# Optimization experiments

Measured on AMD Instinct MI355X. Metric: run time of the kernel, lower is better.

## Reference

```python
import jax, jax.numpy as jnp
import numpy as np

B, N = 1, 4096
DIM, DEPTH, HEADS, DH = 768, 6, 12, 64
INNER = HEADS * DH
FF = 4 * DIM
M = 256            # FAVOR+ random features
NC = 100           # num_classes
VOCAB_OUT = NC + 2
N_POS = 50000


def setup_inputs() -> dict:
    key = jax.random.key(0)
    ks = jax.random.split(key, 16)
    s = 0.02
    d = {}
    d["methy"]  = jax.random.uniform(ks[0], (B, N), jnp.float32)
    d["chromo"] = jax.random.randint(ks[1], (B, N), 0, 30)
    d["pos"]    = jnp.sort(jax.random.randint(ks[2], (B, N), 0, N_POS), axis=-1)
    d["methy_table"]  = s * jax.random.normal(ks[3], (NC + 3, DIM), jnp.float32)
    d["chromo_table"] = s * jax.random.normal(ks[4], (30, DIM), jnp.float32)
    d["pos_table"]    = s * jax.random.normal(ks[5], (N_POS, DIM), jnp.float32)
    d["ln1_g"] = jnp.ones((DEPTH, DIM)); d["ln1_b"] = jnp.zeros((DEPTH, DIM))
    d["ln2_g"] = jnp.ones((DEPTH, DIM)); d["ln2_b"] = jnp.zeros((DEPTH, DIM))
    d["Wq"] = s * jax.random.normal(ks[6], (DEPTH, DIM, INNER), jnp.float32)
    d["Wk"] = s * jax.random.normal(ks[7], (DEPTH, DIM, INNER), jnp.float32)
    d["Wv"] = s * jax.random.normal(ks[8], (DEPTH, DIM, INNER), jnp.float32)
    d["Wo"] = s * jax.random.normal(ks[9], (DEPTH, INNER, DIM), jnp.float32)
    d["bo"] = jnp.zeros((DEPTH, DIM))
    d["W1"] = s * jax.random.normal(ks[10], (DEPTH, DIM, FF), jnp.float32)
    d["b1"] = jnp.zeros((DEPTH, FF))
    d["W2"] = s * jax.random.normal(ks[11], (DEPTH, FF, DIM), jnp.float32)
    d["b2"] = jnp.zeros((DEPTH, DIM))
    d["proj"] = jax.random.normal(ks[12], (DEPTH, M, DH), jnp.float32)  # fixed FAVOR+ projections
    d["normf_g"] = jnp.ones((DIM,)); d["normf_b"] = jnp.zeros((DIM,))
    d["Wout"] = s * jax.random.normal(ks[13], (DIM, VOCAB_OUT), jnp.float32)
    d["bout"] = jnp.zeros((VOCAB_OUT,))
    return d


def layernorm(x, g, b, eps=1e-5):
    mu = jnp.mean(x, -1, keepdims=True)
    var = jnp.var(x, -1, keepdims=True)
    return (x - mu) * jax.lax.rsqrt(var + eps) * g + b


def softmax_kernel(x, proj, is_query, eps=1e-4):
    # FAVOR+ positive random features approximating the softmax kernel.
    dnorm = x.shape[-1] ** -0.25
    ratio = proj.shape[0] ** -0.5
    xn = x * dnorm
    xd = jnp.einsum('bhnd,md->bhnm', xn, proj)            # [b,h,n,m]
    diag = 0.5 * jnp.sum(xn * xn, -1, keepdims=True)
    if is_query:
        mx = jnp.max(xd, axis=-1, keepdims=True)
    else:
        mx = jnp.max(xd, axis=(-2, -1), keepdims=True)
    return ratio * (jnp.exp(xd - diag - mx) + eps)


def favor_attention(x, mask, Wq, Wk, Wv, Wo, bo, proj):
    b, n, _ = x.shape
    def split(h):  # [b,n,inner] -> [b,h,n,d]
        return h.reshape(b, n, HEADS, DH).transpose(0, 2, 1, 3)
    q, k, v = split(x @ Wq), split(x @ Wk), split(x @ Wv)
    qf = softmax_kernel(q, proj, True)
    kf = softmax_kernel(k, proj, False)
    kf = kf * mask[:, None, :, None]                      # zero padded keys
    k_sum = kf.sum(axis=-2)                               # [b,h,m]
    d_inv = 1.0 / jnp.einsum('bhnm,bhm->bhn', qf, k_sum)
    ctx = jnp.einsum('bhnm,bhnd->bhmd', kf, v)            # [b,h,m,d]
    o = jnp.einsum('bhnm,bhmd,bhn->bhnd', qf, ctx, d_inv)
    o = o.transpose(0, 2, 1, 3).reshape(b, n, INNER)
    return o @ Wo + bo


def reference(methy, chromo, pos, methy_table, chromo_table, pos_table,
              ln1_g, ln1_b, ln2_g, ln2_b, Wq, Wk, Wv, Wo, bo,
              W1, b1, W2, b2, proj, normf_g, normf_b, Wout, bout):
    # ContinuousEmbedding (discretized): torch.bucketize(x, boundaries[:-1]) == searchsorted left
    boundaries = jnp.concatenate([jnp.array([-2.0, -1.0], jnp.float32),
                                  jnp.linspace(0.0, 1.0, NC + 1)])
    idx = jnp.searchsorted(boundaries[:-1], methy, side='left')
    mask = methy != 0
    x = methy_table[idx] + pos_table[pos] + chromo_table[chromo]
    for l in range(DEPTH):  # pre-norm Performer blocks
        h = layernorm(x, ln1_g[l], ln1_b[l])
        x = x + favor_attention(h, mask, Wq[l], Wk[l], Wv[l], Wo[l], bo[l], proj[l])
        h = layernorm(x, ln2_g[l], ln2_b[l])
        x = x + jax.nn.gelu(h @ W1[l] + b1[l]) @ W2[l] + b2[l]
    x = layernorm(x, normf_g, normf_b)
    return x @ Wout + bout
```

## Files before the change

kernel.cpp:

```cpp
#include <hip/hip_runtime.h>
#include <cstdint>

typedef __bf16 bf16_t;
typedef __bf16 bf16x8 __attribute__((ext_vector_type(8)));
typedef __bf16 bf16x4 __attribute__((ext_vector_type(4)));
typedef float f32x4 __attribute__((ext_vector_type(4)));

#define NTOK 4096
#define DIM 768
#define DEPTH 6
#define HEADS 12
#define FFD 3072
#define VOUT 102

__device__ __forceinline__ void gl_lds16(const void* g, void* l) {
    __builtin_amdgcn_global_load_lds(
        (__attribute__((address_space(1))) void*)(g),
        (__attribute__((address_space(3))) void*)(l), 16, 0, 0);
}

__device__ __forceinline__ unsigned enc_f32(float f) {
    unsigned u = __float_as_uint(f);
    return (u & 0x80000000u) ? ~u : (u | 0x80000000u);
}
__device__ __forceinline__ float dec_f32(unsigned e) {
    unsigned u = (e & 0x80000000u) ? (e & 0x7FFFFFFFu) : ~e;
    return __uint_as_float(u);
}

template<int MODE>
__global__ __launch_bounds__(256, 2) void gemm128(
    const bf16_t* __restrict__ A, int lda, long sA,
    const bf16_t* __restrict__ B, int ldb, long sB,
    void* __restrict__ Cout, int ldc, long sC,
    int K, int nsplit,
    const float* __restrict__ bias,
    const float* __restrict__ rowscale,
    int Mvalid, int Nvalid, void* __restrict__ aux)
{
    __shared__ __align__(16) bf16_t smem[16896];
    bf16_t* As = smem;
    bf16_t* Bs = smem + 8192;
    const int bz = blockIdx.z;
    const int batch = bz / nsplit, chunk = bz % nsplit;
    A += (long)batch * sA;
    B += (long)batch * sB;
    const int t = threadIdx.x;
    const int wave = t >> 6, lane = t & 63;
    const int wm = wave >> 1, wn = wave & 1;
    const int q = lane >> 4, r = lane & 15;
    const int tileM = blockIdx.x * 128, tileN = blockIdx.y * 128;
    const int Kc = K / nsplit;
    const int k0 = chunk * Kc;

    f32x4 acc[4][4] = {};

    for (int kt = 0; kt < Kc; kt += 64) {
        const int kb = k0 + kt;
#pragma unroll
        for (int i = 0; i < 4; i++) {
            const int c = i * 256 + t;
            const int row = c >> 3, kk = (c & 7) * 8;
            gl_lds16(A + (long)(tileM + row) * lda + kb + kk, (char*)As + (i * 256 + wave * 64) * 16);
            gl_lds16(B + (long)(tileN + row) * ldb + kb + kk, (char*)Bs + (i * 256 + wave * 64) * 16);
        }
        __syncthreads();
#pragma unroll
        for (int kk = 0; kk < 64; kk += 32) {
            bf16x8 af[4], bfr[4];
#pragma unroll
            for (int i = 0; i < 4; i++)
                af[i] = *(const bf16x8*)(As + (wm * 64 + i * 16 + r) * 64 + kk + q * 8);
#pragma unroll
            for (int j = 0; j < 4; j++)
                bfr[j] = *(const bf16x8*)(Bs + (wn * 64 + j * 16 + r) * 64 + kk + q * 8);
#pragma unroll
            for (int i = 0; i < 4; i++)
#pragma unroll
                for (int j = 0; j < 4; j++)
                    acc[i][j] = __builtin_amdgcn_mfma_f32_16x16x32_bf16(af[i], bfr[j], acc[i][j], 0, 0, 0);
        }
        __syncthreads();
    }

    if (MODE == 8) {
        const float dn = 0.3535533905932738f;
        if (tileN < 1536) {
            bf16_t* QK = (bf16_t*)Cout;
            const int hcol = (tileN >> 6) + wn;
            float* dptr = (hcol < 12) ? ((float*)bias + (long)hcol * 4096)
                                      : ((float*)rowscale + (long)(hcol - 12) * 4096);
#pragma unroll
            for (int i = 0; i < 4; i++) {
#pragma unroll
                for (int e = 0; e < 4; e++) {
                    const int R = tileM + wm * 64 + i * 16 + q * 4 + e;
                    float ss = 0.0f;
#pragma unroll
                    for (int j = 0; j < 4; j++) {
                        const int Cc = tileN + wn * 64 + j * 16 + r;
                        const float v = acc[i][j][e] * dn;
                        QK[(long)R * 1536 + Cc] = (bf16_t)v;
                        ss += v * v;
                    }
                    for (int o = 8; o; o >>= 1) ss += __shfl_xor(ss, o);
                    if (r == 0) dptr[R] = 0.5f * ss;
                }
            }
        } else {
            bf16_t* VTp = (bf16_t*)aux;
            bf16_t* tile = smem;
#pragma unroll
            for (int i = 0; i < 4; i++)
#pragma unroll
                for (int j = 0; j < 4; j++)
#pragma unroll
                    for (int e = 0; e < 4; e++) {
                        const int row = wm * 64 + i * 16 + q * 4 + e;
                        const int col = wn * 64 + j * 16 + r;
                        tile[col * 130 + row] = (bf16_t)acc[i][j][e];
                    }
            __syncthreads();
            const int col = t >> 1, half = (t & 1) * 64;
            const int cg = tileN - 1536 + col;
            const int h = cg >> 6, d = cg & 63;
            bf16_t* dst = VTp + ((long)h * 128 + d) * 4096 + tileM + half;
            const bf16_t* src = tile + col * 130 + half;
#pragma unroll
            for (int u2 = 0; u2 < 64; u2 += 8)
                *(bf16x8*)(dst + u2) = *(const bf16x8*)(src + u2);
        }
        return;
    }

#pragma unroll
    for (int i = 0; i < 4; i++) {
#pragma unroll
        for (int j = 0; j < 4; j++) {
#pragma unroll
            for (int e = 0; e < 4; e++) {
                const int R = tileM + wm * 64 + i * 16 + q * 4 + e;
                const int Cc = tileN + wn * 64 + j * 16 + r;
                const float v = acc[i][j][e];
                if (MODE == 2) {
                    const float x = v + bias[Cc];
                    const float z = 0.7978845608028654f * (x + 0.044715f * x * x * x);
                    const float th = 1.0f - 2.0f / (__expf(2.0f * z) + 1.0f);
                    bf16_t* Gp = (bf16_t*)Cout;
                    Gp[(long)R * ldc + Cc] = (bf16_t)(0.5f * x * (1.0f + th));
                } else if (MODE == 4) {
                    if (R < Mvalid) {
                        float* C = (float*)Cout + (long)batch * sC;
                        atomicAdd(&C[(long)R * ldc + Cc], v);
                    }
                } else if (MODE == 5) {
                    if (Cc < Nvalid) {
                        float* C = (float*)Cout;
                        C[(long)R * ldc + Cc] = v + bias[Cc];
                    }
                } else if (MODE == 9) {
                    float* C = (float*)Cout + (long)chunk * sC;
                    C[(long)R * ldc + Cc] = v;
                }
            }
        }
    }
}

__global__ __launch_bounds__(256, 2) void qk_feat(
    const bf16_t* __restrict__ QKbf,
    const bf16_t* __restrict__ projbf,
    const float* __restrict__ diagQ,
    bf16_t* __restrict__ QF,
    unsigned* __restrict__ kmx)
{
    __shared__ __align__(16) bf16_t As[128 * 64];
    __shared__ __align__(16) bf16_t Bs[256 * 64];
    __shared__ float rmax[2][128];
    const int z = blockIdx.y;
    const bool isq = z < 12;
    const int h = isq ? z : z - 12;
    const int tileM = blockIdx.x * 128;
    const int t = threadIdx.x, wave = t >> 6, lane = t & 63;
    const int wm = wave >> 1, wn = wave & 1;
    const int q = lane >> 4, r = lane & 15;
    const bf16_t* A = QKbf + (isq ? 0 : 768) + h * 64;

#pragma unroll
    for (int i = 0; i < 4; i++) {
        const int c = i * 256 + t;
        gl_lds16(A + (long)(tileM + (c >> 3)) * 1536 + (c & 7) * 8, (char*)As + (i * 256 + wave * 64) * 16);
    }
#pragma unroll
    for (int i = 0; i < 8; i++) {
        const int c = i * 256 + t;
        gl_lds16(projbf + c * 8, (char*)Bs + (i * 256 + wave * 64) * 16);
    }
    __syncthreads();

    f32x4 acc[4][8] = {};
#pragma unroll
    for (int kk = 0; kk < 64; kk += 32) {
        bf16x8 af[4], bfr[8];
#pragma unroll
        for (int i = 0; i < 4; i++)
            af[i] = *(const bf16x8*)(As + (wm * 64 + i * 16 + r) * 64 + kk + q * 8);
#pragma unroll
        for (int j = 0; j < 8; j++)
            bfr[j] = *(const bf16x8*)(Bs + (wn * 128 + j * 16 + r) * 64 + kk + q * 8);
#pragma unroll
        for (int i = 0; i < 4; i++)
#pragma unroll
            for (int j = 0; j < 8; j++)
                acc[i][j] = __builtin_amdgcn_mfma_f32_16x16x32_bf16(af[i], bfr[j], acc[i][j], 0, 0, 0);
    }

    if (!isq) {
        float m = -3.0e38f;
#pragma unroll
        for (int i = 0; i < 4; i++)
#pragma unroll
            for (int j = 0; j < 8; j++)
#pragma unroll
                for (int e = 0; e < 4; e++) m = fmaxf(m, acc[i][j][e]);
        for (int o = 32; o; o >>= 1) m = fmaxf(m, __shfl_xor(m, o));
        if (lane == 0) rmax[0][wave] = m;
        __syncthreads();
        if (t == 0) {
            m = fmaxf(fmaxf(rmax[0][0], rmax[0][1]), fmaxf(rmax[0][2], rmax[0][3]));
            atomicMax(kmx + h, enc_f32(m));
        }
        return;
    }

#pragma unroll
    for (int i = 0; i < 4; i++) {
#pragma unroll
        for (int e = 0; e < 4; e++) {
            float m = acc[i][0][e];
#pragma unroll
            for (int j = 1; j < 8; j++) m = fmaxf(m, acc[i][j][e]);
            for (int o = 8; o; o >>= 1) m = fmaxf(m, __shfl_xor(m, o));
            if (r == 0) rmax[wn][wm * 64 + i * 16 + q * 4 + e] = m;
        }
    }
    __syncthreads();
    const float ratio = 0.0625f;
#pragma unroll
    for (int i = 0; i < 4; i++) {
#pragma unroll
        for (int e = 0; e < 4; e++) {
            const int rl = wm * 64 + i * 16 + q * 4 + e;
            const int R = tileM + rl;
            const float dg = diagQ[h * 4096 + R] + fmaxf(rmax[0][rl], rmax[1][rl]);
            bf16_t* op = QF + ((long)h * 4096 + R) * 256 + wn * 128 + r;
#pragma unroll
            for (int j = 0; j < 8; j++)
                op[j * 16] = (bf16_t)(ratio * (__expf(acc[i][j][e] - dg) + 1e-4f));
        }
    }
}

__global__ __launch_bounds__(256, 2) void kfeat_fused(
    const bf16_t* __restrict__ QKbf,
    const bf16_t* __restrict__ projbf,
    const float* __restrict__ diagK,
    const unsigned* __restrict__ kmxe,
    const float* __restrict__ maskf,
    bf16_t* __restrict__ KFT)
{
    __shared__ __align__(16) bf16_t smem[24576];
    bf16_t* As = smem;
    bf16_t* Bs = smem + 8192;
    const int h = blockIdx.y;
    const int tileM = blockIdx.x * 128;
    const int t = threadIdx.x, wave = t >> 6, lane = t & 63;
    const int wm = wave >> 1, wn = wave & 1;
    const int q = lane >> 4, r = lane & 15;
    const bf16_t* A = QKbf + 768 + h * 64;

#pragma unroll
    for (int i = 0; i < 4; i++) {
        const int c = i * 256 + t;
        gl_lds16(A + (long)(tileM + (c >> 3)) * 1536 + (c & 7) * 8, (char*)As + (i * 256 + wave * 64) * 16);
    }
#pragma unroll
    for (int i = 0; i < 8; i++) {
        const int c = i * 256 + t;
        gl_lds16(projbf + c * 8, (char*)Bs + (i * 256 + wave * 64) * 16);
    }
    __syncthreads();

    f32x4 acc[4][8] = {};
#pragma unroll
    for (int kk = 0; kk < 64; kk += 32) {
        bf16x8 af[4], bfr[8];
#pragma unroll
        for (int i = 0; i < 4; i++)
            af[i] = *(const bf16x8*)(As + (wm * 64 + i * 16 + r) * 64 + kk + q * 8);
#pragma unroll
        for (int j = 0; j < 8; j++)
            bfr[j] = *(const bf16x8*)(Bs + (wn * 128 + j * 16 + r) * 64 + kk + q * 8);
#pragma unroll
        for (int i = 0; i < 4; i++)
#pragma unroll
            for (int j = 0; j < 8; j++)
                acc[i][j] = __builtin_amdgcn_mfma_f32_16x16x32_bf16(af[i], bfr[j], acc[i][j], 0, 0, 0);
    }

    const float km = dec_f32(kmxe[h]);
    const float ratio = 0.0625f;
    float dg[4][4], mk[4][4];
#pragma unroll
    for (int i = 0; i < 4; i++)
#pragma unroll
        for (int e = 0; e < 4; e++) {
            const int R = tileM + wm * 64 + i * 16 + q * 4 + e;
            dg[i][e] = diagK[h * 4096 + R] + km;
            mk[i][e] = maskf[R];
        }

    bf16_t* tile = smem;
#pragma unroll
    for (int mhalf = 0; mhalf < 2; mhalf++) {
        __syncthreads();
        if (wn == mhalf) {
#pragma unroll
            for (int i = 0; i < 4; i++)
#pragma unroll
                for (int j = 0; j < 8; j++)
#pragma unroll
                    for (int e = 0; e < 4; e++) {
                        const int rl = wm * 64 + i * 16 + q * 4 + e;
                        const int lc = j * 16 + r;
                        tile[lc * 136 + rl] =
                            (bf16_t)(ratio * (__expf(acc[i][j][e] - dg[i][e]) + 1e-4f) * mk[i][e]);
                    }
        }
        __syncthreads();
        const int m = t >> 1, nb = (t & 1) * 64;
        bf16_t* dst = KFT + ((long)h * 256 + mhalf * 128 + m) * 4096 + tileM + nb;
        const bf16_t* src = tile + m * 136 + nb;
#pragma unroll
        for (int c = 0; c < 64; c += 8)
            *(bf16x8*)(dst + c) = *(const bf16x8*)(src + c);
    }
}

__global__ __launch_bounds__(256, 2) void pv_fused(
    const bf16_t* __restrict__ QF,
    const float* __restrict__ CTXf,
    bf16_t* __restrict__ O)
{
    __shared__ __align__(16) bf16_t As[128 * 64];
    __shared__ __align__(16) bf16_t Bs[80 * 64];
    const int h = blockIdx.y;
    const int tileM = blockIdx.x * 128;
    const int t = threadIdx.x, wave = t >> 6, lane = t & 63;
    const int wm = wave >> 1, wn = wave & 1;
    const int q = lane >> 4, r = lane & 15;

    f32x4 acc[4][5] = {};
    for (int kt = 0; kt < 256; kt += 64) {
#pragma unroll
        for (int i = 0; i < 4; i++) {
            const int c = i * 256 + t;
            gl_lds16(QF + ((long)h * 4096 + tileM + (c >> 3)) * 256 + kt + (c & 7) * 8,
                     (char*)As + (i * 256 + wave * 64) * 16);
        }
#pragma unroll
        for (int u = 0; u < 5; u++) {
            const int idx = u * 256 + t;
            const int row = idx >> 4, c4 = (idx & 15) * 4;
            const float4 v = *(const float4*)(CTXf + ((long)h * 80 + row) * 256 + kt + c4);
            bf16x4 o4; o4[0] = (bf16_t)v.x; o4[1] = (bf16_t)v.y; o4[2] = (bf16_t)v.z; o4[3] = (bf16_t)v.w;
            *(bf16x4*)(Bs + row * 64 + c4) = o4;
        }
        __syncthreads();
#pragma unroll
        for (int kk = 0; kk < 64; kk += 32) {
            bf16x8 af[4], bfr[5];
#pragma unroll
            for (int i = 0; i < 4; i++)
                af[i] = *(const bf16x8*)(As + (wm * 64 + i * 16 + r) * 64 + kk + q * 8);
#pragma unroll
            for (int j = 0; j < 5; j++)
                bfr[j] = *(const bf16x8*)(Bs + ((wn * 0 + j * 16 + r)) * 64 + kk + q * 8);
#pragma unroll
            for (int i = 0; i < 4; i++)
#pragma unroll
                for (int j = 0; j < 5; j++)
                    acc[i][j] = __builtin_amdgcn_mfma_f32_16x16x32_bf16(af[i], bfr[j], acc[i][j], 0, 0, 0);
        }
        __syncthreads();
    }
    if (wn == 1) return;
#pragma unroll
    for (int i = 0; i < 4; i++) {
#pragma unroll
        for (int e = 0; e < 4; e++) {
            const int R = tileM + wm * 64 + i * 16 + q * 4 + e;
            float den = __shfl(acc[i][4][e], lane & 0x30);
            const float dinv = 1.0f / den;
            bf16_t* op = O + (long)R * 768 + h * 64;
#pragma unroll
            for (int j = 0; j < 4; j++)
                op[j * 16 + r] = (bf16_t)(acc[i][j][e] * dinv);
        }
    }
}

__global__ void bucket_kernel(const float* __restrict__ methy, int* __restrict__ idx, float* __restrict__ maskf) {
    const int n = blockIdx.x * 256 + threadIdx.x;
    if (n >= NTOK) return;
    const float u = methy[n];
    int cnt = (int)(u > -2.0f) + (int)(u > -1.0f);
    for (int k = 0; k < 100; k++) cnt += (int)(((float)k * 0.01f) < u);
    idx[n] = cnt;
    maskf[n] = (u != 0.0f) ? 1.0f : 0.0f;
}

__global__ void embed_kernel(const int* __restrict__ idx, const int* __restrict__ pos, const int* __restrict__ chromo,
                             const float* __restrict__ mt, const float* __restrict__ pt, const float* __restrict__ ct,
                             float* __restrict__ X) {
    const int n = blockIdx.x, t = threadIdx.x;
    const float4* a = (const float4*)(mt + (long)idx[n] * DIM);
    const float4* b = (const float4*)(pt + (long)pos[n] * DIM);
    const float4* c = (const float4*)(ct + (long)chromo[n] * DIM);
    float4 rr = a[t];
    const float4 u = b[t], w = c[t];
    rr.x += u.x + w.x; rr.y += u.y + w.y; rr.z += u.z + w.z; rr.w += u.w + w.w;
    ((float4*)(X + (long)n * DIM))[t] = rr;
}

__global__ __launch_bounds__(256) void ln_fused(float* __restrict__ X,
        const float* __restrict__ D0, const float* __restrict__ D1, const float* __restrict__ rb,
        const float* __restrict__ g, const float* __restrict__ b, bf16_t* __restrict__ out) {
    const int n = blockIdx.x, t = threadIdx.x;
    float* x = X + (long)n * DIM;
    float v[3];
#pragma unroll
    for (int j = 0; j < 3; j++) {
        const int c = t + j * 256;
        float xv = x[c];
        if (D0) {
            xv += D0[(long)n * DIM + c] + D1[(long)n * DIM + c] + rb[c];
            x[c] = xv;
        }
        v[j] = xv;
    }
    float s = v[0] + v[1] + v[2];
    float s2 = v[0] * v[0] + v[1] * v[1] + v[2] * v[2];
    __shared__ float smA[4], smB[4];
    for (int o = 32; o; o >>= 1) { s += __shfl_down(s, o); s2 += __shfl_down(s2, o); }
    if ((t & 63) == 0) { smA[t >> 6] = s; smB[t >> 6] = s2; }
    __syncthreads();
    s = smA[0] + smA[1] + smA[2] + smA[3];
    s2 = smB[0] + smB[1] + smB[2] + smB[3];
    const float mu = s * (1.0f / DIM);
    const float var = s2 * (1.0f / DIM) - mu * mu;
    const float rs = rsqrtf(var + 1e-5f);
    bf16_t* op = out + (long)n * DIM;
#pragma unroll
    for (int j = 0; j < 3; j++) {
        const int c = t + j * 256;
        op[c] = (bf16_t)((v[j] - mu) * rs * g[c] + b[c]);
    }
}

__global__ __launch_bounds__(256) void transpose4(const float* __restrict__ Wq, const float* __restrict__ Wk,
        const float* __restrict__ Wv, const float* __restrict__ Wo,
        bf16_t* __restrict__ WqkvT, bf16_t* __restrict__ WoT) {
    __shared__ float tile[32][33];
    const int z = blockIdx.z, l = z >> 2, j = z & 3;
    const float* in = (j == 0 ? Wq : j == 1 ? Wk : j == 2 ? Wv : Wo) + (long)l * 768 * 768;
    bf16_t* out = (j < 3) ? WqkvT + (long)l * 2304 * 768 + (long)j * 768 * 768
                          : WoT + (long)l * 768 * 768;
    const int c0 = blockIdx.x * 32, r0 = blockIdx.y * 32;
    const int t = threadIdx.x, tx = t & 31, ty = t >> 5;
    for (int i = 0; i < 32; i += 8)
        tile[ty + i][tx] = in[(long)(r0 + ty + i) * 768 + c0 + tx];
    __syncthreads();
    for (int i = 0; i < 32; i += 8)
        out[(long)(c0 + ty + i) * 768 + r0 + tx] = (bf16_t)tile[tx][ty + i];
}

__global__ __launch_bounds__(256) void transpose_b(const float* __restrict__ in, long sIn, int R, int C,
                                                   bf16_t* __restrict__ out, long sOut, int ldo) {
    __shared__ float tile[32][33];
    in += (long)blockIdx.z * sIn;
    out += (long)blockIdx.z * sOut;
    const int c0 = blockIdx.x * 32, r0 = blockIdx.y * 32;
    const int t = threadIdx.x, tx = t & 31, ty = t >> 5;
    for (int i = 0; i < 32; i += 8) {
        const int rr = r0 + ty + i, cc = c0 + tx;
        tile[ty + i][tx] = (rr < R && cc < C) ? in[(long)rr * C + cc] : 0.0f;
    }
    __syncthreads();
    for (int i = 0; i < 32; i += 8) {
        const int cc = c0 + ty + i, rr = r0 + tx;
        if (cc < C && rr < R) out[(long)cc * ldo + rr] = (bf16_t)tile[tx][ty + i];
    }
}

__global__ void conv_kernel(const float* __restrict__ in, bf16_t* __restrict__ out, long n) {
    const long i = ((long)blockIdx.x * 256 + threadIdx.x) * 4;
    if (i >= n) return;
    const float4 v = *(const float4*)(in + i);
    bf16x4 o; o[0] = (bf16_t)v.x; o[1] = (bf16_t)v.y; o[2] = (bf16_t)v.z; o[3] = (bf16_t)v.w;
    *(bf16x4*)(out + i) = o;
}

__global__ void vtones_kernel(bf16_t* __restrict__ VT) {
    const int i = blockIdx.x * 256 + threadIdx.x;
    const int h = i >> 12, n = i & 4095;
    VT[((long)h * 128 + 64) * 4096 + n] = (bf16_t)1.0f;
}

extern "C" void kernel_launch(void* const* d_in, const int* in_sizes, int n_in,
                              void* d_out, int out_size, void* d_ws, size_t ws_size,
                              hipStream_t stream) {
    const float* methy        = (const float*)d_in[0];
    const int*   chromo       = (const int*)d_in[1];
    const int*   pos          = (const int*)d_in[2];
    const float* methy_table  = (const float*)d_in[3];
    const float* chromo_table = (const float*)d_in[4];
    const float* pos_table    = (const float*)d_in[5];
    const float* ln1_g = (const float*)d_in[6];
    const float* ln1_b = (const float*)d_in[7];
    const float* ln2_g = (const float*)d_in[8];
    const float* ln2_b = (const float*)d_in[9];
    const float* Wq = (const float*)d_in[10];
    const float* Wk = (const float*)d_in[11];
    const float* Wv = (const float*)d_in[12];
    const float* Wo = (const float*)d_in[13];
    const float* bo = (const float*)d_in[14];
    const float* W1 = (const float*)d_in[15];
    const float* b1 = (const float*)d_in[16];
    const float* W2 = (const float*)d_in[17];
    const float* b2 = (const float*)d_in[18];
    const float* proj = (const float*)d_in[19];
    const float* normf_g = (const float*)d_in[20];
    const float* normf_b = (const float*)d_in[21];
    const float* Wout = (const float*)d_in[22];
    const float* bout = (const float*)d_in[23];

    char* p = (char*)d_ws;
    auto alloc = [&](size_t bytes) { char* r = p; p += (bytes + 255) & ~(size_t)255; return r; };

    float*  X     = (float*)alloc((size_t)NTOK * DIM * 4);
    bf16_t* Hbf   = (bf16_t*)alloc((size_t)NTOK * DIM * 2);
    bf16_t* G     = (bf16_t*)alloc((size_t)NTOK * FFD * 2);
    float*  D     = (float*)alloc((size_t)2 * NTOK * DIM * 4);
    bf16_t* QKbf  = (bf16_t*)alloc((size_t)NTOK * 1536 * 2);
    bf16_t* O     = QKbf;
    bf16_t* VT    = (bf16_t*)alloc((size_t)12 * 128 * 4096 * 2);
    bf16_t* QF    = (bf16_t*)alloc((size_t)12 * 4096 * 256 * 2);
    bf16_t* KFT   = (bf16_t*)alloc((size_t)12 * 256 * 4096 * 2);
    bf16_t* WqkvT = (bf16_t*)alloc((size_t)DEPTH * 2304 * 768 * 2);
    bf16_t* WoT   = (bf16_t*)alloc((size_t)DEPTH * 768 * 768 * 2);
    bf16_t* W1T   = (bf16_t*)alloc((size_t)DEPTH * 3072 * 768 * 2);
    bf16_t* W2T   = (bf16_t*)alloc((size_t)DEPTH * 768 * 3072 * 2);
    bf16_t* projbf= (bf16_t*)alloc((size_t)DEPTH * 256 * 64 * 2);
    bf16_t* WoutT = (bf16_t*)alloc((size_t)128 * 768 * 2);
    float*  diagQ = (float*)alloc((size_t)12 * 4096 * 4);
    float*  diagK = (float*)alloc((size_t)12 * 4096 * 4);
    const size_t ZB_CTX = (size_t)12 * 80 * 256 * 4;
    char*   ZERO  = alloc(ZB_CTX + 64);
    float*  CTXf  = (float*)ZERO;
    unsigned* kmx = (unsigned*)(ZERO + ZB_CTX);
    int*    idxb  = (int*)alloc((size_t)4096 * 4);
    float*  maskf = (float*)alloc((size_t)4096 * 4);

    hipMemsetAsync(VT, 0, (size_t)12 * 128 * 4096 * 2, stream);
    hipMemsetAsync(WoutT, 0, (size_t)128 * 768 * 2, stream);
    vtones_kernel<<<192, 256, 0, stream>>>(VT);

    bucket_kernel<<<16, 256, 0, stream>>>(methy, idxb, maskf);
    embed_kernel<<<4096, 192, 0, stream>>>(idxb, pos, chromo, methy_table, pos_table, chromo_table, X);

    const long s768 = (long)768 * 768, sQKV = (long)2304 * 768, sFF = (long)3072 * 768;
    transpose4<<<dim3(24, 24, 4 * DEPTH), 256, 0, stream>>>(Wq, Wk, Wv, Wo, WqkvT, WoT);
    transpose_b<<<dim3(96, 24, DEPTH), 256, 0, stream>>>(W1, sFF, 768, 3072, W1T, sFF, 768);
    transpose_b<<<dim3(24, 96, DEPTH), 256, 0, stream>>>(W2, sFF, 3072, 768, W2T, sFF, 3072);
    transpose_b<<<dim3(4, 24, 1), 256, 0, stream>>>(Wout, 0, 768, VOUT, WoutT, 0, 768);
    conv_kernel<<<96, 256, 0, stream>>>(proj, projbf, (long)DEPTH * 256 * 64);

    float* D0 = D;
    float* D1 = D + (long)NTOK * DIM;

    for (int l = 0; l < DEPTH; l++) {
        const bf16_t* lWqkv = WqkvT + (long)l * sQKV;
        const bf16_t* lWo   = WoT + (long)l * s768;
        const bf16_t* lW1   = W1T + (long)l * sFF;
        const bf16_t* lW2   = W2T + (long)l * sFF;
        const bf16_t* lproj = projbf + (long)l * 256 * 64;

        hipMemsetAsync(ZERO, 0, ZB_CTX + 64, stream);

        if (l == 0)
            ln_fused<<<4096, 256, 0, stream>>>(X, nullptr, nullptr, nullptr,
                                               ln1_g, ln1_b, Hbf);
        else
            ln_fused<<<4096, 256, 0, stream>>>(X, D0, D1, b2 + (l - 1) * DIM,
                                               ln1_g + l * DIM, ln1_b + l * DIM, Hbf);

        gemm128<8><<<dim3(32, 18, 1), 256, 0, stream>>>(Hbf, 768, 0, lWqkv, 768, 0, QKbf, 1536, 0,
                                                        768, 1, diagQ, diagK, 4096, 2304, VT);
        qk_feat<<<dim3(32, 24), 256, 0, stream>>>(QKbf, lproj, diagQ, QF, kmx);
        kfeat_fused<<<dim3(32, 12), 256, 0, stream>>>(QKbf, lproj, diagK, kmx, maskf, KFT);

        gemm128<4><<<dim3(1, 2, 96), 256, 0, stream>>>(VT, 4096, (long)128 * 4096, KFT, 4096, (long)256 * 4096,
                                                       CTXf, 256, (long)80 * 256, 4096, 8,
                                                       nullptr, nullptr, 65, 256, nullptr);
        pv_fused<<<dim3(32, 12), 256, 0, stream>>>(QF, CTXf, O);

        gemm128<9><<<dim3(32, 6, 2), 256, 0, stream>>>(O, 768, 0, lWo, 768, 0, D, 768, (long)NTOK * DIM,
                                                       768, 2, nullptr, nullptr, 4096, 768, nullptr);
        ln_fused<<<4096, 256, 0, stream>>>(X, D0, D1, bo + l * DIM,
                                           ln2_g + l * DIM, ln2_b + l * DIM, Hbf);
        gemm128<2><<<dim3(32, 24, 1), 256, 0, stream>>>(Hbf, 768, 0, lW1, 768, 0, G, 3072, 0,
                                                        768, 1, b1 + l * FFD, nullptr, 4096, 3072, nullptr);
        gemm128<9><<<dim3(32, 6, 2), 256, 0, stream>>>(G, 3072, 0, lW2, 3072, 0, D, 768, (long)NTOK * DIM,
                                                       3072, 2, nullptr, nullptr, 4096, 768, nullptr);
    }

    ln_fused<<<4096, 256, 0, stream>>>(X, D0, D1, b2 + (DEPTH - 1) * DIM, normf_g, normf_b, Hbf);
    gemm128<5><<<dim3(32, 1, 1), 256, 0, stream>>>(Hbf, 768, 0, WoutT, 768, 0, d_out, VOUT, 0,
                                                   768, 1, bout, nullptr, 4096, VOUT, nullptr);
}
```

Before: 1.638 ms.

## Store split-K partials in bf16, drop per-layer memsets, widen PV tiles

Split-K partial outputs for the Wo and W2 GEMMs are now written in bf16 instead of fp32, which halves the write and re-read traffic in the residual layernorm. The context GEMM now writes per-chunk partials that pv_fused sums itself, replacing atomics and the per-layer memset. kmx is initialised inside the QKV GEMM. pv_fused moves to 256-row tiles so all four waves do useful work. The final projection becomes a split-K atomic GEMM over a pre-zeroed output. Storing the residual partials in bf16 adds rounding error to the residual stream.

```diff
diff --git a/kernel.cpp b/kernel.cpp
--- a/kernel.cpp
+++ b/kernel.cpp
@@ -84,6 +84,10 @@
     }
 
     if (MODE == 8) {
+        if (blockIdx.x == 0 && blockIdx.y == 0 && t < 12) {
+            unsigned* kmx = (unsigned*)((bf16_t*)aux + (long)12 * 128 * 4096);
+            kmx[t] = enc_f32(-3.0e38f);
+        }
         const float dn = 0.3535533905932738f;
         if (tileN < 1536) {
             bf16_t* QK = (bf16_t*)Cout;
@@ -149,18 +153,18 @@
                     bf16_t* Gp = (bf16_t*)Cout;
                     Gp[(long)R * ldc + Cc] = (bf16_t)(0.5f * x * (1.0f + th));
                 } else if (MODE == 4) {
-                    if (R < Mvalid) {
-                        float* C = (float*)Cout + (long)batch * sC;
-                        atomicAdd(&C[(long)R * ldc + Cc], v);
-                    }
-                } else if (MODE == 5) {
                     if (Cc < Nvalid) {
                         float* C = (float*)Cout;
-                        C[(long)R * ldc + Cc] = v + bias[Cc];
+                        atomicAdd(&C[(long)R * ldc + Cc], v + (chunk == 0 ? bias[Cc] : 0.0f));
                     }
                 } else if (MODE == 9) {
-                    float* C = (float*)Cout + (long)chunk * sC;
-                    C[(long)R * ldc + Cc] = v;
+                    if (R < Mvalid) {
+                        float* C = (float*)Cout + (long)bz * sC;
+                        C[(long)R * ldc + Cc] = v;
+                    }
+                } else if (MODE == 10) {
+                    bf16_t* C = (bf16_t*)Cout + (long)bz * sC;
+                    C[(long)R * ldc + Cc] = (bf16_t)v;
                 }
             }
         }
@@ -349,21 +353,20 @@
 
 __global__ __launch_bounds__(256, 2) void pv_fused(
     const bf16_t* __restrict__ QF,
-    const float* __restrict__ CTXf,
+    const float* __restrict__ CTXc,
     bf16_t* __restrict__ O)
 {
-    __shared__ __align__(16) bf16_t As[128 * 64];
+    __shared__ __align__(16) bf16_t As[256 * 64];
     __shared__ __align__(16) bf16_t Bs[80 * 64];
     const int h = blockIdx.y;
-    const int tileM = blockIdx.x * 128;
+    const int tileM = blockIdx.x * 256;
     const int t = threadIdx.x, wave = t >> 6, lane = t & 63;
-    const int wm = wave >> 1, wn = wave & 1;
     const int q = lane >> 4, r = lane & 15;
 
     f32x4 acc[4][5] = {};
     for (int kt = 0; kt < 256; kt += 64) {
 #pragma unroll
-        for (int i = 0; i < 4; i++) {
+        for (int i = 0; i < 8; i++) {
             const int c = i * 256 + t;
             gl_lds16(QF + ((long)h * 4096 + tileM + (c >> 3)) * 256 + kt + (c & 7) * 8,
                      (char*)As + (i * 256 + wave * 64) * 16);
@@ -372,8 +375,13 @@
         for (int u = 0; u < 5; u++) {
             const int idx = u * 256 + t;
             const int row = idx >> 4, c4 = (idx & 15) * 4;
-            const float4 v = *(const float4*)(CTXf + ((long)h * 80 + row) * 256 + kt + c4);
-            bf16x4 o4; o4[0] = (bf16_t)v.x; o4[1] = (bf16_t)v.y; o4[2] = (bf16_t)v.z; o4[3] = (bf16_t)v.w;
+            float4 s = {0.f, 0.f, 0.f, 0.f};
+#pragma unroll
+            for (int ch = 0; ch < 8; ch++) {
+                const float4 v = *(const float4*)(CTXc + ((long)(h * 8 + ch) * 80 + row) * 256 + kt + c4);
+                s.x += v.x; s.y += v.y; s.z += v.z; s.w += v.w;
+            }
+            bf16x4 o4; o4[0] = (bf16_t)s.x; o4[1] = (bf16_t)s.y; o4[2] = (bf16_t)s.z; o4[3] = (bf16_t)s.w;
             *(bf16x4*)(Bs + row * 64 + c4) = o4;
         }
         __syncthreads();
@@ -382,10 +390,10 @@
             bf16x8 af[4], bfr[5];
 #pragma unroll
             for (int i = 0; i < 4; i++)
-                af[i] = *(const bf16x8*)(As + (wm * 64 + i * 16 + r) * 64 + kk + q * 8);
+                af[i] = *(const bf16x8*)(As + (wave * 64 + i * 16 + r) * 64 + kk + q * 8);
 #pragma unroll
             for (int j = 0; j < 5; j++)
-                bfr[j] = *(const bf16x8*)(Bs + ((wn * 0 + j * 16 + r)) * 64 + kk + q * 8);
+                bfr[j] = *(const bf16x8*)(Bs + (j * 16 + r) * 64 + kk + q * 8);
 #pragma unroll
             for (int i = 0; i < 4; i++)
 #pragma unroll
@@ -394,13 +402,12 @@
         }
         __syncthreads();
     }
-    if (wn == 1) return;
 #pragma unroll
     for (int i = 0; i < 4; i++) {
 #pragma unroll
         for (int e = 0; e < 4; e++) {
-            const int R = tileM + wm * 64 + i * 16 + q * 4 + e;
-            float den = __shfl(acc[i][4][e], lane & 0x30);
+            const int R = tileM + wave * 64 + i * 16 + q * 4 + e;
+            const float den = __shfl(acc[i][4][e], lane & 0x30);
             const float dinv = 1.0f / den;
             bf16_t* op = O + (long)R * 768 + h * 64;
 #pragma unroll
@@ -434,7 +441,7 @@
 }
 
 __global__ __launch_bounds__(256) void ln_fused(float* __restrict__ X,
-        const float* __restrict__ D0, const float* __restrict__ D1, const float* __restrict__ rb,
+        const bf16_t* __restrict__ D0, const bf16_t* __restrict__ D1, const float* __restrict__ rb,
         const float* __restrict__ g, const float* __restrict__ b, bf16_t* __restrict__ out) {
     const int n = blockIdx.x, t = threadIdx.x;
     float* x = X + (long)n * DIM;
@@ -444,7 +451,7 @@
         const int c = t + j * 256;
         float xv = x[c];
         if (D0) {
-            xv += D0[(long)n * DIM + c] + D1[(long)n * DIM + c] + rb[c];
+            xv += (float)D0[(long)n * DIM + c] + (float)D1[(long)n * DIM + c] + rb[c];
             x[c] = xv;
         }
         v[j] = xv;
@@ -551,10 +558,11 @@
     float*  X     = (float*)alloc((size_t)NTOK * DIM * 4);
     bf16_t* Hbf   = (bf16_t*)alloc((size_t)NTOK * DIM * 2);
     bf16_t* G     = (bf16_t*)alloc((size_t)NTOK * FFD * 2);
-    float*  D     = (float*)alloc((size_t)2 * NTOK * DIM * 4);
+    bf16_t* D     = (bf16_t*)alloc((size_t)2 * NTOK * DIM * 2);
     bf16_t* QKbf  = (bf16_t*)alloc((size_t)NTOK * 1536 * 2);
     bf16_t* O     = QKbf;
     bf16_t* VT    = (bf16_t*)alloc((size_t)12 * 128 * 4096 * 2);
+    unsigned* kmx = (unsigned*)alloc(64);
     bf16_t* QF    = (bf16_t*)alloc((size_t)12 * 4096 * 256 * 2);
     bf16_t* KFT   = (bf16_t*)alloc((size_t)12 * 256 * 4096 * 2);
     bf16_t* WqkvT = (bf16_t*)alloc((size_t)DEPTH * 2304 * 768 * 2);
@@ -565,15 +573,13 @@
     bf16_t* WoutT = (bf16_t*)alloc((size_t)128 * 768 * 2);
     float*  diagQ = (float*)alloc((size_t)12 * 4096 * 4);
     float*  diagK = (float*)alloc((size_t)12 * 4096 * 4);
-    const size_t ZB_CTX = (size_t)12 * 80 * 256 * 4;
-    char*   ZERO  = alloc(ZB_CTX + 64);
-    float*  CTXf  = (float*)ZERO;
-    unsigned* kmx = (unsigned*)(ZERO + ZB_CTX);
+    float*  CTXc  = (float*)alloc((size_t)12 * 8 * 80 * 256 * 4);
     int*    idxb  = (int*)alloc((size_t)4096 * 4);
     float*  maskf = (float*)alloc((size_t)4096 * 4);
 
     hipMemsetAsync(VT, 0, (size_t)12 * 128 * 4096 * 2, stream);
     hipMemsetAsync(WoutT, 0, (size_t)128 * 768 * 2, stream);
+    hipMemsetAsync(d_out, 0, (size_t)out_size * 4, stream);
     vtones_kernel<<<192, 256, 0, stream>>>(VT);
 
     bucket_kernel<<<16, 256, 0, stream>>>(methy, idxb, maskf);
@@ -586,8 +592,8 @@
     transpose_b<<<dim3(4, 24, 1), 256, 0, stream>>>(Wout, 0, 768, VOUT, WoutT, 0, 768);
     conv_kernel<<<96, 256, 0, stream>>>(proj, projbf, (long)DEPTH * 256 * 64);
 
-    float* D0 = D;
-    float* D1 = D + (long)NTOK * DIM;
+    bf16_t* D0 = D;
+    bf16_t* D1 = D + (long)NTOK * DIM;
 
     for (int l = 0; l < DEPTH; l++) {
         const bf16_t* lWqkv = WqkvT + (long)l * sQKV;
@@ -596,11 +602,8 @@
         const bf16_t* lW2   = W2T + (long)l * sFF;
         const bf16_t* lproj = projbf + (long)l * 256 * 64;
 
-        hipMemsetAsync(ZERO, 0, ZB_CTX + 64, stream);
-
         if (l == 0)
-            ln_fused<<<4096, 256, 0, stream>>>(X, nullptr, nullptr, nullptr,
-                                               ln1_g, ln1_b, Hbf);
+            ln_fused<<<4096, 256, 0, stream>>>(X, nullptr, nullptr, nullptr, ln1_g, ln1_b, Hbf);
         else
             ln_fused<<<4096, 256, 0, stream>>>(X, D0, D1, b2 + (l - 1) * DIM,
                                                ln1_g + l * DIM, ln1_b + l * DIM, Hbf);
@@ -610,22 +613,22 @@
         qk_feat<<<dim3(32, 24), 256, 0, stream>>>(QKbf, lproj, diagQ, QF, kmx);
         kfeat_fused<<<dim3(32, 12), 256, 0, stream>>>(QKbf, lproj, diagK, kmx, maskf, KFT);
 
-        gemm128<4><<<dim3(1, 2, 96), 256, 0, stream>>>(VT, 4096, (long)128 * 4096, KFT, 4096, (long)256 * 4096,
-                                                       CTXf, 256, (long)80 * 256, 4096, 8,
-                                                       nullptr, nullptr, 65, 256, nullptr);
-        pv_fused<<<dim3(32, 12), 256, 0, stream>>>(QF, CTXf, O);
-
-        gemm128<9><<<dim3(32, 6, 2), 256, 0, stream>>>(O, 768, 0, lWo, 768, 0, D, 768, (long)NTOK * DIM,
-                                                       768, 2, nullptr, nullptr, 4096, 768, nullptr);
+        gemm128<9><<<dim3(1, 2, 96), 256, 0, stream>>>(VT, 4096, (long)128 * 4096, KFT, 4096, (long)256 * 4096,
+                                                       CTXc, 256, (long)80 * 256, 4096, 8,
+                                                       nullptr, nullptr, 80, 256, nullptr);
+        pv_fused<<<dim3(16, 12), 256, 0, stream>>>(QF, CTXc, O);
+
+        gemm128<10><<<dim3(32, 6, 2), 256, 0, stream>>>(O, 768, 0, lWo, 768, 0, D, 768, (long)NTOK * DIM,
+                                                        768, 2, nullptr, nullptr, 4096, 768, nullptr);
         ln_fused<<<4096, 256, 0, stream>>>(X, D0, D1, bo + l * DIM,
                                            ln2_g + l * DIM, ln2_b + l * DIM, Hbf);
         gemm128<2><<<dim3(32, 24, 1), 256, 0, stream>>>(Hbf, 768, 0, lW1, 768, 0, G, 3072, 0,
                                                         768, 1, b1 + l * FFD, nullptr, 4096, 3072, nullptr);
-        gemm128<9><<<dim3(32, 6, 2), 256, 0, stream>>>(G, 3072, 0, lW2, 3072, 0, D, 768, (long)NTOK * DIM,
-                                                       3072, 2, nullptr, nullptr, 4096, 768, nullptr);
+        gemm128<10><<<dim3(32, 6, 2), 256, 0, stream>>>(G, 3072, 0, lW2, 3072, 0, D, 768, (long)NTOK * DIM,
+                                                        3072, 2, nullptr, nullptr, 4096, 768, nullptr);
     }
 
     ln_fused<<<4096, 256, 0, stream>>>(X, D0, D1, b2 + (DEPTH - 1) * DIM, normf_g, normf_b, Hbf);
-    gemm128<5><<<dim3(32, 1, 1), 256, 0, stream>>>(Hbf, 768, 0, WoutT, 768, 0, d_out, VOUT, 0,
-                                                   768, 1, bout, nullptr, 4096, VOUT, nullptr);
-}
+    gemm128<4><<<dim3(32, 1, 4), 256, 0, stream>>>(Hbf, 768, 0, WoutT, 768, 0, d_out, VOUT, 0,
+                                                   768, 4, bout, nullptr, 4096, VOUT, nullptr);
+}
```

After: 1.825 ms. 1.11x slower.
